# Performance work log

Hardware: AMD Instinct MI355X
Metric: run time of the kernel (lower is better)

Reference implementation:

```python
import jax, jax.numpy as jnp
import numpy as np

B, T, D, H = 4, 1024, 1024, 16
DK = D // H
SCALE = float(np.sqrt(DK))


def setup_inputs() -> dict:
    key = jax.random.key(0)
    ks = jax.random.split(key, 12)
    std = 1.0 / np.sqrt(D)
    inp = {
        "x": jax.random.normal(ks[0], (B, T, D), dtype=jnp.float32),
        "s2_distances": jax.random.uniform(ks[1], (B, T, T), dtype=jnp.float32),
        # causal mask: 1 where attention allowed (j <= i)
        "mask": jnp.broadcast_to(jnp.tril(jnp.ones((T, T), dtype=jnp.int32)), (B, T, T)),
        "Wq": jax.random.uniform(ks[2], (D, D), jnp.float32, -std, std),
        "bq": jax.random.uniform(ks[3], (D,), jnp.float32, -std, std),
        "Wk": jax.random.uniform(ks[4], (D, D), jnp.float32, -std, std),
        "bk": jax.random.uniform(ks[5], (D,), jnp.float32, -std, std),
        "Wv": jax.random.uniform(ks[6], (D, D), jnp.float32, -std, std),
        "bv": jax.random.uniform(ks[7], (D,), jnp.float32, -std, std),
        "Wo": jax.random.uniform(ks[8], (D, D), jnp.float32, -std, std),
        "bo": jax.random.uniform(ks[9], (D,), jnp.float32, -std, std),
        "spatial_weight": jnp.float32(0.5),
    }
    return inp


def reference(x, s2_distances, mask, Wq, bq, Wk, bk, Wv, bv, Wo, bo, spatial_weight):
    b, t, _ = x.shape
    # projections: torch nn.Linear is x @ W.T + b
    def proj(W, bias):
        y = jnp.einsum("btd,ed->bte", x, W) + bias
        return y.reshape(b, t, H, DK).transpose(0, 2, 1, 3)  # [B,H,T,dk]

    Q, K, V = proj(Wq, bq), proj(Wk, bk), proj(Wv, bv)
    # scores: QK^T/sqrt(dk) - |alpha| * dist  (dist broadcast over heads)
    scores = jnp.einsum("bhqd,bhkd->bhqk", Q, K) / SCALE
    scores = scores - jnp.abs(spatial_weight) * s2_distances[:, None, :, :]
    scores = jnp.where(mask[:, None, :, :] == 0, -jnp.inf, scores)
    probs = jax.nn.softmax(scores, axis=-1)
    out = jnp.einsum("bhqk,bhkd->bhqd", probs, V)
    out = out.transpose(0, 2, 1, 3).reshape(b, t, D)
    return jnp.einsum("btd,ed->bte", out, Wo) + bo
```

## Files before the change

kernel.cpp:

```cpp
#include <hip/hip_runtime.h>
#include <stdint.h>

#define Tt 1024
#define Dd 1024
#define Hh 16

typedef unsigned short u16;
typedef __attribute__((ext_vector_type(8))) short short8;
typedef __attribute__((ext_vector_type(4))) float f32x4;
typedef __attribute__((ext_vector_type(4))) unsigned short u16x4;

typedef const __attribute__((address_space(1))) uint32_t* gptr_t;
typedef __attribute__((address_space(3))) uint32_t* lptr_t;

#define QSCALE 0.18033688011112042f
#define LOG2E 1.4426950408889634f

static __device__ __forceinline__ u16 f2bf(float f) {
  union { float f; unsigned u; } x;
  x.f = f;
  unsigned u = x.u;
  return (u16)((u + 0x7fffu + ((u >> 16) & 1u)) >> 16);
}

static __device__ __forceinline__ u16 f2bf_fast(float f) {
  union { float f; unsigned u; } x;
  x.f = f;
  return (u16)((x.u + 0x8000u) >> 16);
}

static __device__ __forceinline__ float bf2f(u16 u) {
  union { unsigned u; float f; } x;
  x.u = ((unsigned)u) << 16;
  return x.f;
}

static __device__ __forceinline__ float fexp2(float x) {
#if __has_builtin(__builtin_amdgcn_exp2f)
  return __builtin_amdgcn_exp2f(x);
#else
  return exp2f(x);
#endif
}

__global__ __launch_bounds__(256) void cvt_kernel(
    const float* __restrict__ x, const float* __restrict__ wq,
    const float* __restrict__ wk, const float* __restrict__ wv,
    const float* __restrict__ wo, const float* __restrict__ dist,
    const float* __restrict__ alphap, u16* __restrict__ xb,
    u16* __restrict__ wb, u16* __restrict__ biasb) {
  size_t i = ((size_t)blockIdx.x * 256 + threadIdx.x) * 4;
  const size_t XN = (size_t)4 * 1024 * 1024;
  const size_t WN = (size_t)8 * 1024 * 1024;
  float mul = 1.0f;
  const float* src;
  u16* dst;
  size_t off;
  if (i < XN) {
    src = x; dst = xb; off = i;
  } else if (i < WN) {
    size_t j = i - XN;
    int wi = (int)(j >> 20);
    src = (wi == 0) ? wq : (wi == 1) ? wk : (wi == 2) ? wv : wo;
    dst = wb + ((size_t)wi << 20);
    off = j & ((1u << 20) - 1);
  } else {
    src = dist; dst = biasb; off = i - WN;
    mul = -fabsf(alphap[0]) * LOG2E;
  }
  float4 v = *(const float4*)(src + off);
  u16x4 o;
  o.x = f2bf(v.x * mul); o.y = f2bf(v.y * mul);
  o.z = f2bf(v.z * mul); o.w = f2bf(v.w * mul);
  *(u16x4*)(dst + off) = o;
}

__global__ __launch_bounds__(512, 2) void qkv_fused_kernel(
    const u16* __restrict__ xb, const u16* __restrict__ wb,
    const float* __restrict__ bq, const float* __restrict__ bk,
    const float* __restrict__ bv, u16* __restrict__ Q, u16* __restrict__ Kk,
    u16* __restrict__ Vt) {
  __shared__ u16 lds[65536];
  const int bid = blockIdx.x;
  const int mt = bid & 15, ny = bid >> 4;
  const int z = ny >> 2;
  const int m0 = mt * 256, nc = (ny & 3) * 256;
  const u16* W = wb + ((size_t)z << 20);

  const int t = threadIdx.x, w = t >> 6, l = t & 63;
  const int quad = l >> 4, l15 = l & 15;
  const int wr = w >> 2, wn = w & 3;
  char* ldc = (char*)lds;

  const int srow = t >> 3;
  const int schunk = ((t & 7) ^ (srow & 7)) * 8;
  const u16* gA = xb + (size_t)(m0 + srow) * Dd + schunk;
  const u16* gB = W + (size_t)(nc + srow) * Dd + schunk;
  const int lb = w * 1024;

  auto stage = [&](int kt, int buf) {
#pragma unroll
    for (int u = 0; u < 4; u++) {
      __builtin_amdgcn_global_load_lds(
          (gptr_t)(gA + (size_t)u * 64 * Dd + kt * 64),
          (lptr_t)(ldc + buf * 65536 + u * 8192 + lb), 16, 0, 0);
      __builtin_amdgcn_global_load_lds(
          (gptr_t)(gB + (size_t)u * 64 * Dd + kt * 64),
          (lptr_t)(ldc + buf * 65536 + 32768 + u * 8192 + lb), 16, 0, 0);
    }
  };

  f32x4 acc[8][4];
#pragma unroll
  for (int i = 0; i < 8; i++)
#pragma unroll
    for (int j = 0; j < 4; j++) acc[i][j] = (f32x4){0.f, 0.f, 0.f, 0.f};

  stage(0, 0);
  asm volatile("s_waitcnt vmcnt(0)" ::: "memory");
  __builtin_amdgcn_s_barrier();

  const int xr = l15 & 7;

#pragma unroll 1
  for (int kt = 0; kt < 16; kt++) {
    const int buf = kt & 1;
    const char* sl = ldc + buf * 65536;
    if (kt + 1 < 16) stage(kt + 1, buf ^ 1);
#pragma unroll
    for (int ks = 0; ks < 2; ks++) {
      short8 af[8], bfv[4];
      const int cs = ((ks * 4 + quad) ^ xr) * 16;
#pragma unroll
      for (int mi = 0; mi < 8; mi++)
        af[mi] = *(const short8*)(sl + (wr * 128 + mi * 16 + l15) * 128 + cs);
#pragma unroll
      for (int ni = 0; ni < 4; ni++)
        bfv[ni] = *(const short8*)(sl + 32768 + (wn * 64 + ni * 16 + l15) * 128 + cs);
      __builtin_amdgcn_s_barrier();
      asm volatile("s_waitcnt lgkmcnt(0)" ::: "memory");
      __builtin_amdgcn_sched_barrier(0);
      __builtin_amdgcn_s_setprio(1);
#pragma unroll
      for (int mi = 0; mi < 8; mi++)
#pragma unroll
        for (int ni = 0; ni < 4; ni++)
          acc[mi][ni] = __builtin_amdgcn_mfma_f32_16x16x32_bf16(
              af[mi], bfv[ni], acc[mi][ni], 0, 0, 0);
      __builtin_amdgcn_s_setprio(0);
      if (ks == 1) asm volatile("s_waitcnt vmcnt(0)" ::: "memory");
      __builtin_amdgcn_s_barrier();
    }
  }

  const float* bias = (z == 0) ? bq : (z == 1) ? bk : bv;
  const float scl = (z == 0) ? QSCALE : 1.0f;
  if (z < 2) {
#pragma unroll
    for (int mi = 0; mi < 8; mi++)
#pragma unroll
      for (int ni = 0; ni < 4; ni++) {
        const int n = wn * 64 + ni * 16 + l15;
        const float bn = bias[nc + n];
        const int nsw = n ^ (quad << 4);
#pragma unroll
        for (int r = 0; r < 4; r++) {
          const int m = wr * 128 + mi * 16 + quad * 4 + r;
          lds[m * 256 + nsw] = f2bf((acc[mi][ni][r] + bn) * scl);
        }
      }
  } else {
#pragma unroll
    for (int mi = 0; mi < 8; mi++)
#pragma unroll
      for (int ni = 0; ni < 4; ni++) {
        const int n = wn * 64 + ni * 16 + l15;
        const float bn = bias[nc + n];
        u16x4 o;
        o.x = f2bf(acc[mi][ni][0] + bn);
        o.y = f2bf(acc[mi][ni][1] + bn);
        o.z = f2bf(acc[mi][ni][2] + bn);
        o.w = f2bf(acc[mi][ni][3] + bn);
        const int mp = (wr * 128 + mi * 16 + quad * 4) ^ ((n & 7) * 8);
        *(u16x4*)&lds[n * 256 + mp] = o;
      }
  }
  __syncthreads();
  const int row = t >> 5;
  const int c8 = (t & 31) * 8;
  if (z < 2) {
    u16* out = (z == 0) ? Q : Kk;
#pragma unroll
    for (int it = 0; it < 16; it++) {
      const int rr = it * 16 + row;
      const int pos = c8 ^ ((((rr >> 2) & 3)) << 4);
      *(short8*)(out + (size_t)(m0 + rr) * Dd + nc + c8) =
          *(const short8*)&lds[rr * 256 + pos];
    }
  } else {
    const int b2 = m0 >> 10, t0 = m0 & (Tt - 1);
#pragma unroll
    for (int it = 0; it < 16; it++) {
      const int rr = it * 16 + row;
      const int pos = c8 ^ ((rr & 7) * 8);
      *(short8*)(Vt + ((size_t)b2 * Dd + nc + rr) * Tt + t0 + c8) =
          *(const short8*)&lds[rr * 256 + pos];
    }
  }
}

__global__ __launch_bounds__(512) void gemm_out_kernel(
    const u16* __restrict__ Ao, const u16* __restrict__ Wo,
    const float* __restrict__ bo, float* __restrict__ out) {
  __shared__ u16 lds[2 * 12288];
  const int m0 = blockIdx.x * 128, n0 = blockIdx.y * 64;
  const int t = threadIdx.x, w = t >> 6, l = t & 63, quad = l >> 4, l15 = l & 15;
  const int srow = t >> 3;
  const int scol = ((l & 7) ^ ((l >> 3) & 7)) * 8;
  const u16* ga = Ao + (size_t)(m0 + srow) * Dd + scol;
  const u16* gb = Wo + (size_t)(n0 + srow) * Dd + scol;
  char* ldc = (char*)lds;
  const int xr = l15 & 7;
  f32x4 acc[4];
#pragma unroll
  for (int j = 0; j < 4; j++) acc[j] = (f32x4){0.f, 0.f, 0.f, 0.f};

  auto stage = [&](int k0, int buf) {
    char* base = ldc + buf * 24576 + w * 1024;
#pragma unroll
    for (int i = 0; i < 2; i++)
      __builtin_amdgcn_global_load_lds((gptr_t)(ga + k0 + (size_t)i * 64 * Dd),
                                       (lptr_t)(base + i * 8192), 16, 0, 0);
    __builtin_amdgcn_global_load_lds((gptr_t)(gb + k0),
                                     (lptr_t)(base + 16384), 16, 0, 0);
  };

  stage(0, 0);
#pragma unroll 1
  for (int it = 0; it < Dd / 64; it++) {
    const int buf = it & 1;
    __builtin_amdgcn_s_waitcnt(0);
    __syncthreads();
    if (it + 1 < Dd / 64) stage((it + 1) * 64, buf ^ 1);
    const u16* lA = lds + buf * 12288;
    const u16* lB = lA + 8192;
#pragma unroll
    for (int kk = 0; kk < 2; kk++) {
      const int cs = ((kk * 4 + quad) ^ xr) * 8;
      const short8 af = *(const short8*)(lA + (w * 16 + l15) * 64 + cs);
#pragma unroll
      for (int ni = 0; ni < 4; ni++) {
        const short8 bfr = *(const short8*)(lB + (ni * 16 + l15) * 64 + cs);
        acc[ni] = __builtin_amdgcn_mfma_f32_16x16x32_bf16(af, bfr, acc[ni], 0, 0, 0);
      }
    }
  }
#pragma unroll
  for (int ni = 0; ni < 4; ni++) {
    const int n = n0 + ni * 16 + l15;
    const float bn = bo[n];
#pragma unroll
    for (int r = 0; r < 4; r++) {
      const int m = m0 + w * 16 + quad * 4 + r;
      out[(size_t)m * Dd + n] = acc[ni][r] + bn;
    }
  }
}

__global__ __launch_bounds__(256) void attn_kernel(
    const u16* __restrict__ Q, const u16* __restrict__ Kk,
    const u16* __restrict__ Vt, const u16* __restrict__ biasb,
    u16* __restrict__ Oo) {
  __shared__ u16 lK[2][64 * 64];
  __shared__ u16 lV[2][64 * 64];
  __shared__ u16 lPp[4][16 * 64];
  const int t = threadIdx.x, w = t >> 6, l = t & 63, quad = l >> 4, l15 = l & 15;
  const int g = blockIdx.x >> 8;
  const int j = (blockIdx.x >> 6) & 3;
  const int bh = blockIdx.x & 63;
  const int qb = (g == 0) ? 15 - j : (g == 1) ? 8 + j : (g == 2) ? 7 - j : j;
  const int h = bh & (Hh - 1), b = bh >> 4;
  const int q0 = qb * 64;

  const int srow = w * 8 + (l >> 3);
  const int schunk = ((l & 7) ^ ((l >> 3) & 7)) * 8;
  const u16* gK = Kk + ((size_t)b * Tt + srow) * Dd + h * 64 + schunk;
  const u16* gV = Vt + ((size_t)b * Dd + h * 64 + srow) * Tt + schunk;
  char* lKc0 = (char*)&lK[0][0];
  char* lVc0 = (char*)&lV[0][0];
  const int wbase = w * 1024;

  auto stage = [&](int k0, int buf) {
#pragma unroll
    for (int i = 0; i < 2; i++) {
      __builtin_amdgcn_global_load_lds(
          (gptr_t)(gK + (size_t)(k0 + i * 32) * Dd),
          (lptr_t)(lKc0 + buf * 8192 + wbase + i * 4096), 16, 0, 0);
      __builtin_amdgcn_global_load_lds(
          (gptr_t)(gV + (size_t)(i * 32) * Tt + k0),
          (lptr_t)(lVc0 + buf * 8192 + wbase + i * 4096), 16, 0, 0);
    }
  };

  const int qrow = q0 + w * 16 + l15;
  const u16* Qp = Q + ((size_t)b * Tt + qrow) * Dd + h * 64 + quad * 8;
  const short8 qf0 = *(const short8*)Qp;
  const short8 qf1 = *(const short8*)(Qp + 32);
  const u16* bp = biasb + ((size_t)b * Tt + qrow) * Tt + quad * 4;

  const int xr = l15 & 7;
  u16* lpr = &lPp[w][l15 * 64];
  const int niter = qb + 1;

  f32x4 oacc[4];
#pragma unroll
  for (int dt = 0; dt < 4; dt++) oacc[dt] = (f32x4){0.f, 0.f, 0.f, 0.f};
  f32x4 lsum4 = (f32x4){0.f, 0.f, 0.f, 0.f};
  u16x4 bbA[4], bbB[4];

  stage(0, 0);
#pragma unroll
  for (int nt = 0; nt < 4; nt++) bbA[nt] = *(const u16x4*)(bp + nt * 16);

#pragma unroll 1
  for (int kt = 0; kt < niter; kt++) {
    const int buf = kt & 1;
    __builtin_amdgcn_s_waitcnt(0);
    __syncthreads();
    if (kt + 1 < niter) {
      stage((kt + 1) * 64, buf ^ 1);
#pragma unroll
      for (int nt = 0; nt < 4; nt++)
        bbB[nt] = *(const u16x4*)(bp + (kt + 1) * 64 + nt * 16);
    }
    f32x4 sacc[4];
#pragma unroll
    for (int nt = 0; nt < 4; nt++) {
#pragma unroll
      for (int r = 0; r < 4; r++) sacc[nt][r] = bf2f(bbA[nt][r]);
    }
#pragma unroll
    for (int ks = 0; ks < 2; ks++) {
      const short8 qf = ks ? qf1 : qf0;
      const int cs = ((ks * 4 + quad) ^ xr) * 8;
#pragma unroll
      for (int nt = 0; nt < 4; nt++) {
        const short8 kf = *(const short8*)&lK[buf][(nt * 16 + l15) * 64 + cs];
        sacc[nt] = __builtin_amdgcn_mfma_f32_16x16x32_bf16(kf, qf, sacc[nt], 0, 0, 0);
      }
    }
    if (kt == qb) {
      const int kbase = kt * 64 + quad * 4;
#pragma unroll
      for (int nt = 0; nt < 4; nt++) {
        u16x4 pk;
#pragma unroll
        for (int r = 0; r < 4; r++) {
          const float p = (kbase + nt * 16 + r <= qrow) ? fexp2(sacc[nt][r]) : 0.f;
          lsum4[nt] += p;
          pk[r] = f2bf_fast(p);
        }
        *(u16x4*)&lpr[((nt * 4 + quad) ^ (xr << 1)) * 4] = pk;
      }
    } else {
#pragma unroll
      for (int nt = 0; nt < 4; nt++) {
        u16x4 pk;
#pragma unroll
        for (int r = 0; r < 4; r++) {
          const float p = fexp2(sacc[nt][r]);
          lsum4[nt] += p;
          pk[r] = f2bf_fast(p);
        }
        *(u16x4*)&lpr[((nt * 4 + quad) ^ (xr << 1)) * 4] = pk;
      }
    }
#pragma unroll
    for (int ks = 0; ks < 2; ks++) {
      const int cs = ((ks * 4 + quad) ^ xr) * 8;
      const short8 pa = *(const short8*)&lpr[cs];
#pragma unroll
      for (int dt = 0; dt < 4; dt++) {
        const short8 vf = *(const short8*)&lV[buf][(dt * 16 + l15) * 64 + cs];
        oacc[dt] = __builtin_amdgcn_mfma_f32_16x16x32_bf16(pa, vf, oacc[dt], 0, 0, 0);
      }
    }
#pragma unroll
    for (int nt = 0; nt < 4; nt++) bbA[nt] = bbB[nt];
  }

  float lsum = (lsum4[0] + lsum4[1]) + (lsum4[2] + lsum4[3]);
  lsum += __shfl_xor(lsum, 16);
  lsum += __shfl_xor(lsum, 32);
  const float inv = 1.0f / lsum;
  float invq[4];
#pragma unroll
  for (int r = 0; r < 4; r++) invq[r] = __shfl(inv, quad * 4 + r);
#pragma unroll
  for (int dt = 0; dt < 4; dt++) {
#pragma unroll
    for (int r = 0; r < 4; r++) {
      Oo[((size_t)b * Tt + q0 + w * 16 + quad * 4 + r) * Dd + h * 64 + dt * 16 + l15] =
          f2bf(oacc[dt][r] * invq[r]);
    }
  }
}

extern "C" void kernel_launch(void* const* d_in, const int* in_sizes, int n_in,
                              void* d_out, int out_size, void* d_ws, size_t ws_size,
                              hipStream_t stream) {
  const float* x = (const float*)d_in[0];
  const float* dist = (const float*)d_in[1];
  const float* Wq = (const float*)d_in[3];
  const float* bq = (const float*)d_in[4];
  const float* Wk = (const float*)d_in[5];
  const float* bk = (const float*)d_in[6];
  const float* Wv = (const float*)d_in[7];
  const float* bv = (const float*)d_in[8];
  const float* Wo = (const float*)d_in[9];
  const float* bo = (const float*)d_in[10];
  const float* alphap = (const float*)d_in[11];

  char* ws = (char*)d_ws;
  u16* xb = (u16*)(ws);
  u16* wb = (u16*)(ws + ((size_t)8 << 20));
  u16* Qb = (u16*)(ws + ((size_t)16 << 20));
  u16* Kb = (u16*)(ws + ((size_t)24 << 20));
  u16* Vtb = (u16*)(ws + ((size_t)32 << 20));
  u16* biasb = (u16*)(ws + ((size_t)40 << 20));
  u16* Ob = xb;
  float* outp = (float*)d_out;

  cvt_kernel<<<12288, 256, 0, stream>>>(x, Wq, Wk, Wv, Wo, dist, alphap,
                                        xb, wb, biasb);
  qkv_fused_kernel<<<192, 512, 0, stream>>>(xb, wb, bq, bk, bv, Qb, Kb, Vtb);
  attn_kernel<<<1024, 256, 0, stream>>>(Qb, Kb, Vtb, biasb, Ob);
  dim3 g2(32, 16);
  gemm_out_kernel<<<g2, 512, 0, stream>>>(Ob, wb + ((size_t)3 << 20), bo, outp);
}
```

Before: 197.8 us.

## Overlap distance-bias conversion with QKV GEMM and deepen its load pipeline

Moves the conversion of the distance matrix to a scaled bf16 bias out of the elementwise conversion kernel and into 64 extra blocks of the QKV GEMM launch. The 192 GEMM blocks use only part of the device, so that bandwidth-bound work can run on idle CUs alongside them. The GEMM's LDS staging is also restructured: each k-tile is split into two 128-row halves, prefetch runs two tiles ahead, and the loads are issued mid-iteration with partial vmcnt waits. The cost is more complex wait/barrier bookkeeping, and the extra blocks may contend for memory bandwidth with the GEMM.

```diff
diff --git a/kernel.cpp b/kernel.cpp
--- a/kernel.cpp
+++ b/kernel.cpp
@@ -46,32 +46,24 @@
 __global__ __launch_bounds__(256) void cvt_kernel(
     const float* __restrict__ x, const float* __restrict__ wq,
     const float* __restrict__ wk, const float* __restrict__ wv,
-    const float* __restrict__ wo, const float* __restrict__ dist,
-    const float* __restrict__ alphap, u16* __restrict__ xb,
-    u16* __restrict__ wb, u16* __restrict__ biasb) {
+    const float* __restrict__ wo, u16* __restrict__ xb, u16* __restrict__ wb) {
   size_t i = ((size_t)blockIdx.x * 256 + threadIdx.x) * 4;
   const size_t XN = (size_t)4 * 1024 * 1024;
-  const size_t WN = (size_t)8 * 1024 * 1024;
-  float mul = 1.0f;
   const float* src;
   u16* dst;
   size_t off;
   if (i < XN) {
     src = x; dst = xb; off = i;
-  } else if (i < WN) {
+  } else {
     size_t j = i - XN;
     int wi = (int)(j >> 20);
     src = (wi == 0) ? wq : (wi == 1) ? wk : (wi == 2) ? wv : wo;
     dst = wb + ((size_t)wi << 20);
     off = j & ((1u << 20) - 1);
-  } else {
-    src = dist; dst = biasb; off = i - WN;
-    mul = -fabsf(alphap[0]) * LOG2E;
   }
   float4 v = *(const float4*)(src + off);
   u16x4 o;
-  o.x = f2bf(v.x * mul); o.y = f2bf(v.y * mul);
-  o.z = f2bf(v.z * mul); o.w = f2bf(v.w * mul);
+  o.x = f2bf(v.x); o.y = f2bf(v.y); o.z = f2bf(v.z); o.w = f2bf(v.w);
   *(u16x4*)(dst + off) = o;
 }
 
@@ -79,9 +71,25 @@
     const u16* __restrict__ xb, const u16* __restrict__ wb,
     const float* __restrict__ bq, const float* __restrict__ bk,
     const float* __restrict__ bv, u16* __restrict__ Q, u16* __restrict__ Kk,
-    u16* __restrict__ Vt) {
+    u16* __restrict__ Vt, const float* __restrict__ dist,
+    const float* __restrict__ alphap, u16* __restrict__ biasb) {
   __shared__ u16 lds[65536];
   const int bid = blockIdx.x;
+  if (bid >= 192) {
+    const int cid = bid - 192;
+    const float scl = -fabsf(alphap[0]) * LOG2E;
+    const size_t id = (size_t)cid * 512 + threadIdx.x;
+#pragma unroll 4
+    for (int i = 0; i < 32; i++) {
+      const size_t off = id * 4 + (size_t)i * 131072;
+      float4 v = *(const float4*)(dist + off);
+      u16x4 o;
+      o.x = f2bf(v.x * scl); o.y = f2bf(v.y * scl);
+      o.z = f2bf(v.z * scl); o.w = f2bf(v.w * scl);
+      *(u16x4*)(biasb + off) = o;
+    }
+    return;
+  }
   const int mt = bid & 15, ny = bid >> 4;
   const int z = ny >> 2;
   const int m0 = mt * 256, nc = (ny & 3) * 256;
@@ -92,21 +100,20 @@
   const int wr = w >> 2, wn = w & 3;
   char* ldc = (char*)lds;
 
-  const int srow = t >> 3;
-  const int schunk = ((t & 7) ^ (srow & 7)) * 8;
+  const int srow = w * 16 + ((l >> 3) & 7);
+  const int schunk = ((l & 7) ^ ((l >> 3) & 7)) * 8;
   const u16* gA = xb + (size_t)(m0 + srow) * Dd + schunk;
   const u16* gB = W + (size_t)(nc + srow) * Dd + schunk;
-  const int lb = w * 1024;
-
-  auto stage = [&](int kt, int buf) {
-#pragma unroll
-    for (int u = 0; u < 4; u++) {
-      __builtin_amdgcn_global_load_lds(
-          (gptr_t)(gA + (size_t)u * 64 * Dd + kt * 64),
-          (lptr_t)(ldc + buf * 65536 + u * 8192 + lb), 16, 0, 0);
-      __builtin_amdgcn_global_load_lds(
-          (gptr_t)(gB + (size_t)u * 64 * Dd + kt * 64),
-          (lptr_t)(ldc + buf * 65536 + 32768 + u * 8192 + lb), 16, 0, 0);
+
+  auto stage = [&](int kt, int h) {
+    const size_t ro = (size_t)(h * 128) * Dd + (size_t)kt * 64;
+    char* base = ldc + ((((kt & 1) << 1) | h) * 32768) + w * 2048;
+#pragma unroll
+    for (int i = 0; i < 2; i++) {
+      __builtin_amdgcn_global_load_lds((gptr_t)(gA + ro + (size_t)i * 8 * Dd),
+                                       (lptr_t)(base + i * 1024), 16, 0, 0);
+      __builtin_amdgcn_global_load_lds((gptr_t)(gB + ro + (size_t)i * 8 * Dd),
+                                       (lptr_t)(base + 16384 + i * 1024), 16, 0, 0);
     }
   };
 
@@ -116,27 +123,27 @@
 #pragma unroll
     for (int j = 0; j < 4; j++) acc[i][j] = (f32x4){0.f, 0.f, 0.f, 0.f};
 
-  stage(0, 0);
-  asm volatile("s_waitcnt vmcnt(0)" ::: "memory");
+  stage(0, 0); stage(0, 1);
+  stage(1, 0); stage(1, 1);
+  asm volatile("s_waitcnt vmcnt(8)" ::: "memory");
   __builtin_amdgcn_s_barrier();
 
-  const int xr = l15 & 7;
+  const int swl = l15 & 7;
 
 #pragma unroll 1
   for (int kt = 0; kt < 16; kt++) {
-    const int buf = kt & 1;
-    const char* sl = ldc + buf * 65536;
-    if (kt + 1 < 16) stage(kt + 1, buf ^ 1);
-#pragma unroll
-    for (int ks = 0; ks < 2; ks++) {
+    const char* slA = ldc + ((((kt & 1) << 1) | wr) * 32768);
+    const char* slB = ldc + ((((kt & 1) << 1) | (wn >> 1)) * 32768) + 16384;
+    const int rB = (wn & 1) * 64;
+    {
       short8 af[8], bfv[4];
-      const int cs = ((ks * 4 + quad) ^ xr) * 16;
+      const int cs = ((0 * 4 + quad) ^ swl) * 16;
 #pragma unroll
       for (int mi = 0; mi < 8; mi++)
-        af[mi] = *(const short8*)(sl + (wr * 128 + mi * 16 + l15) * 128 + cs);
+        af[mi] = *(const short8*)(slA + (mi * 16 + l15) * 128 + cs);
 #pragma unroll
       for (int ni = 0; ni < 4; ni++)
-        bfv[ni] = *(const short8*)(sl + 32768 + (wn * 64 + ni * 16 + l15) * 128 + cs);
+        bfv[ni] = *(const short8*)(slB + (rB + ni * 16 + l15) * 128 + cs);
       __builtin_amdgcn_s_barrier();
       asm volatile("s_waitcnt lgkmcnt(0)" ::: "memory");
       __builtin_amdgcn_sched_barrier(0);
@@ -148,8 +155,34 @@
           acc[mi][ni] = __builtin_amdgcn_mfma_f32_16x16x32_bf16(
               af[mi], bfv[ni], acc[mi][ni], 0, 0, 0);
       __builtin_amdgcn_s_setprio(0);
-      if (ks == 1) asm volatile("s_waitcnt vmcnt(0)" ::: "memory");
+    }
+    {
+      short8 af[8], bfv[4];
+      const int cs = ((1 * 4 + quad) ^ swl) * 16;
+#pragma unroll
+      for (int mi = 0; mi < 8; mi++)
+        af[mi] = *(const short8*)(slA + (mi * 16 + l15) * 128 + cs);
+#pragma unroll
+      for (int ni = 0; ni < 4; ni++)
+        bfv[ni] = *(const short8*)(slB + (rB + ni * 16 + l15) * 128 + cs);
       __builtin_amdgcn_s_barrier();
+      if (kt + 2 < 16) { stage(kt + 2, 0); stage(kt + 2, 1); }
+      asm volatile("s_waitcnt lgkmcnt(0)" ::: "memory");
+      __builtin_amdgcn_sched_barrier(0);
+      __builtin_amdgcn_s_setprio(1);
+#pragma unroll
+      for (int mi = 0; mi < 8; mi++)
+#pragma unroll
+        for (int ni = 0; ni < 4; ni++)
+          acc[mi][ni] = __builtin_amdgcn_mfma_f32_16x16x32_bf16(
+              af[mi], bfv[ni], acc[mi][ni], 0, 0, 0);
+      __builtin_amdgcn_s_setprio(0);
+      if (kt < 14) {
+        asm volatile("s_waitcnt vmcnt(8)" ::: "memory");
+      } else if (kt == 14) {
+        asm volatile("s_waitcnt vmcnt(0)" ::: "memory");
+      }
+      if (kt < 15) __builtin_amdgcn_s_barrier();
     }
   }
 
@@ -431,9 +464,9 @@
   u16* Ob = xb;
   float* outp = (float*)d_out;
 
-  cvt_kernel<<<12288, 256, 0, stream>>>(x, Wq, Wk, Wv, Wo, dist, alphap,
-                                        xb, wb, biasb);
-  qkv_fused_kernel<<<192, 512, 0, stream>>>(xb, wb, bq, bk, bv, Qb, Kb, Vtb);
+  cvt_kernel<<<8192, 256, 0, stream>>>(x, Wq, Wk, Wv, Wo, xb, wb);
+  qkv_fused_kernel<<<256, 512, 0, stream>>>(xb, wb, bq, bk, bv, Qb, Kb, Vtb,
+                                            dist, alphap, biasb);
   attn_kernel<<<1024, 256, 0, stream>>>(Qb, Kb, Vtb, biasb, Ob);
   dim3 g2(32, 16);
   gemm_out_kernel<<<g2, 512, 0, stream>>>(Ob, wb + ((size_t)3 << 20), bo, outp);
```

Measured after the change: 191.3 us (median of 2 runs). 3.3% less time.
